# Performance work log

Measured on AMD Instinct MI355X. Metric: run time of the kernel, lower is better.

Reference implementation:

```python
import jax, jax.numpy as jnp
import numpy as np

N_QUBITS = 12
N_LAYERS = 2
B, T, IN, H = 256, 32, 8, 128
TWO_PI = 2.0 * np.pi


def _apply_1q(state, U, w):
    # state: (B, 2,2,...,2) with N_QUBITS qubit axes; U: (2,2) or (B,2,2)
    s = jnp.moveaxis(state, w + 1, 1)
    if U.ndim == 3:
        s = jnp.einsum('bst,bt...->bs...', U, s)
    else:
        s = jnp.einsum('st,bt...->bs...', U, s)
    return jnp.moveaxis(s, 1, w + 1)


def _rx_batched(angles):
    # angles: (B,) -> (B,2,2) RX matrices
    c = jnp.cos(angles / 2).astype(jnp.complex64)
    s = jnp.sin(angles / 2).astype(jnp.complex64)
    row0 = jnp.stack([c, -1j * s], axis=-1)
    row1 = jnp.stack([-1j * s, c], axis=-1)
    return jnp.stack([row0, row1], axis=1)


def _rot(phi, theta, omega):
    # PennyLane Rot = RZ(omega) RY(theta) RZ(phi)
    c = jnp.cos(theta / 2).astype(jnp.complex64)
    s = jnp.sin(theta / 2).astype(jnp.complex64)
    ep = jnp.exp(-0.5j * (phi + omega).astype(jnp.complex64))
    em = jnp.exp(-0.5j * (phi - omega).astype(jnp.complex64))
    m00 = ep * c
    m01 = -jnp.conj(em) * s
    m10 = em * s
    m11 = jnp.conj(ep) * c
    return jnp.stack([jnp.stack([m00, m01]), jnp.stack([m10, m11])])


def _cnot(state, cw, tw):
    flipped = jnp.flip(state, axis=tw + 1)
    mask = jnp.arange(2).reshape([2 if a == cw + 1 else 1 for a in range(N_QUBITS + 1)])
    return jnp.where(mask == 1, flipped, state)


def _run_circuit(angles, qw):
    # angles: (B, N_QUBITS) embedding angles; qw: (L, N, 3)
    b = angles.shape[0]
    state = jnp.zeros((b, 2 ** N_QUBITS), jnp.complex64).at[:, 0].set(1.0)
    state = state.reshape((b,) + (2,) * N_QUBITS)
    for w in range(N_QUBITS):  # AngleEmbedding, rotation='X'
        state = _apply_1q(state, _rx_batched(angles[:, w]), w)
    for l in range(N_LAYERS):  # StronglyEntanglingLayers
        for w in range(N_QUBITS):
            state = _apply_1q(state, _rot(qw[l, w, 0], qw[l, w, 1], qw[l, w, 2]), w)
        r = (l % (N_QUBITS - 1)) + 1
        for w in range(N_QUBITS):
            state = _cnot(state, w, (w + r) % N_QUBITS)
    probs = state.real ** 2 + state.imag ** 2
    evs = []
    for i in range(4):  # <Z_i>
        sign = (1.0 - 2.0 * jnp.arange(2, dtype=probs.dtype)).reshape(
            [2 if a == i + 1 else 1 for a in range(N_QUBITS + 1)])
        evs.append(jnp.sum(probs * sign, axis=tuple(range(1, N_QUBITS + 1))))
    return jnp.stack(evs, axis=1)  # (B, 4)


def setup_inputs() -> dict:
    key = jax.random.key(0)
    ks = jax.random.split(key, 12)
    inp = {
        'x': jax.random.normal(ks[0], (B, T, IN), jnp.float32),
        'h0': jnp.zeros((B, H), jnp.float32),
        'c0': jnp.zeros((B, H), jnp.float32),
        'q_weights': jax.random.uniform(ks[1], (N_LAYERS, N_QUBITS, 3), jnp.float32) * TWO_PI,
        'Wf': jax.random.normal(ks[2], (H, 1), jnp.float32),
        'bf': jax.random.normal(ks[3], (H,), jnp.float32) * 0.1,
        'Wi': jax.random.normal(ks[4], (H, 1), jnp.float32),
        'bi': jax.random.normal(ks[5], (H,), jnp.float32) * 0.1,
        'Wc': jax.random.normal(ks[6], (H, 1), jnp.float32),
        'bc': jax.random.normal(ks[7], (H,), jnp.float32) * 0.1,
        'Wo': jax.random.normal(ks[8], (H, 1), jnp.float32),
        'bo': jax.random.normal(ks[9], (H,), jnp.float32) * 0.1,
    }
    return inp


def reference(x, h0, c0, q_weights, Wf, bf, Wi, bi, Wc, bc, Wo, bo):
    def step(carry, x_t):
        h, c = carry
        comb = jnp.concatenate([x_t, h], axis=1)[:, :N_QUBITS]  # truncate, matches source
        q = _run_circuit(comb, q_weights)  # (B, 4) expvals in [-1, 1]
        f = jax.nn.sigmoid(q[:, 0:1] @ Wf.T + bf)
        i = jax.nn.sigmoid(q[:, 1:2] @ Wi.T + bi)
        ct = jnp.tanh(q[:, 2:3] @ Wc.T + bc)
        o = jax.nn.sigmoid(q[:, 3:4] @ Wo.T + bo)
        c_new = f * c + i * ct
        h_new = o * jnp.tanh(c_new)
        return (h_new, c_new), None

    (h_t, c_t), _ = jax.lax.scan(step, (h0, c0), jnp.swapaxes(x, 0, 1))
    return h_t, c_t
```

## Files before the change

### kernel.cpp

```cpp
#include <hip/hip_runtime.h>
#include <math.h>

#define NQ 12
#define NS 4096
#define TT 32
#define BB 256
#define HH 128
#define NT 512

typedef float v2f __attribute__((ext_vector_type(2)));
typedef float v4f __attribute__((ext_vector_type(4)));

constexpr unsigned cnot_g(unsigned x, int w, int r){
    int pc = 11 - w;
    int pt = 11 - ((w + r) % 12);
    return x ^ (((x >> pc) & 1u) << pt);
}
constexpr unsigned Fperm(unsigned i, int r){
    unsigned x = i;
    for (int w = 11; w >= 0; --w) x = cnot_g(x, w, r);
    return x;
}
constexpr unsigned Finv(unsigned i, int r){
    unsigned x = i;
    for (int w = 0; w < 12; ++w) x = cnot_g(x, w, r);
    return x;
}
constexpr unsigned F0closed(unsigned i){
    return i ^ ((i >> 1) & 0x7FFu) ^ ((i & 1u) << 10) ^ ((i & 1u) << 11);
}
constexpr bool check_all(){
    for (int b = 0; b < NQ; ++b){
        const unsigned e = 1u << b;
        if (F0closed(e) != Fperm(e,1)) return false;
        if (Fperm(Finv(e,1),1) != e) return false;
        if (Fperm(Finv(e,2),2) != e) return false;
    }
    if (F0closed(0u) != 0u || Fperm(0u,1) != 0u || Finv(0u,2) != 0u) return false;
    if (F0closed(0x5A3u) != Fperm(0x5A3u,1)) return false;
    if (Fperm(Finv(0xABCu,2),2) != 0xABCu) return false;
    return true;
}
static_assert(check_all(), "CNOT permutation closed forms wrong");
constexpr unsigned maskM(int k){
    unsigned m = 0;
    for (int b = 0; b < NQ; ++b) m |= ((Finv(1u<<b, 2) >> (11 - k)) & 1u) << b;
    return m;
}
constexpr unsigned gM0 = maskM(0), gM1 = maskM(1), gM2 = maskM(2), gM3 = maskM(3);
constexpr int sgn9(unsigned M, int K){ return __builtin_popcount((unsigned)K & (M >> 9)) & 1; }

__device__ __forceinline__ v2f pk_cmul(v2f m, v2f a){
    v2f t;
    asm("v_pk_mul_f32 %0, %1, %2 op_sel:[0,0] op_sel_hi:[0,1]"
        : "=v"(t) : "v"(m), "v"(a));
    asm("v_pk_fma_f32 %0, %1, %2, %0 op_sel:[1,1,0] op_sel_hi:[1,0,1] neg_lo:[1,0,0]"
        : "+v"(t) : "v"(m), "v"(a));
    return t;
}
template<int NL, int NH>
__device__ __forceinline__ void pk_accsgn(v2f &acc, v2f ppb){
    if constexpr (NL==0 && NH==0)
        asm("v_pk_add_f32 %0, %1, %0" : "+v"(acc) : "v"(ppb));
    else if constexpr (NL==1 && NH==0)
        asm("v_pk_add_f32 %0, %1, %0 neg_lo:[1,0]" : "+v"(acc) : "v"(ppb));
    else if constexpr (NL==0 && NH==1)
        asm("v_pk_add_f32 %0, %1, %0 neg_hi:[1,0]" : "+v"(acc) : "v"(ppb));
    else
        asm("v_pk_add_f32 %0, %1, %0 neg_lo:[1,0] neg_hi:[1,0]" : "+v"(acc) : "v"(ppb));
}
template<int K>
__device__ __forceinline__ void expk(const v2f* amp, v2f &a01, v2f &a23){
    const float pp = fmaf(amp[K].x, amp[K].x, amp[K].y * amp[K].y);
    v2f ppb; ppb.x = pp; ppb.y = pp;
    pk_accsgn<sgn9(gM0,K), sgn9(gM1,K)>(a01, ppb);
    pk_accsgn<sgn9(gM2,K), sgn9(gM3,K)>(a23, ppb);
    if constexpr (K < 7) expk<K+1>(amp, a01, a23);
}

template<int C>
__device__ __forceinline__ float dppadd(float v){
    return v + __int_as_float(
        __builtin_amdgcn_update_dpp(0, __float_as_int(v), C, 0xF, 0xF, true));
}
__device__ __forceinline__ float wsum(float v){
    v = dppadd<0x111>(v);
    v = dppadd<0x112>(v);
    v = dppadd<0x114>(v);
    v = dppadd<0x118>(v);
    v = dppadd<0x142>(v);
    v = dppadd<0x143>(v);
    return v;
}
template<int CTRL>
__device__ __forceinline__ float qpermf(float v){
    return __int_as_float(
        __builtin_amdgcn_update_dpp(0, __float_as_int(v), CTRL, 0xF, 0xF, true));
}
template<int CTRL>
__device__ __forceinline__ v4f qperm4(v4f v){
    v4f r;
    r.x = qpermf<CTRL>(v.x); r.y = qpermf<CTRL>(v.y);
    r.z = qpermf<CTRL>(v.z); r.w = qpermf<CTRL>(v.w);
    return r;
}


__device__ __forceinline__ float fsig(float xv){ return __fdividef(1.f, 1.f + __expf(-xv)); }
__device__ __forceinline__ float ftanh(float xv){
    const float e = __expf(-2.f * xv);
    return __fdividef(1.f - e, 1.f + e);
}

template<int WTOP>
__device__ __forceinline__ void rot3ry(v2f* s, const v2f* G){
    #pragma unroll
    for (int lb = 0; lb < 3; ++lb){
        const float cw = G[WTOP-lb].x, sw = G[WTOP-lb].y;
        #pragma unroll
        for (int k = 0; k < 8; ++k){
            if (k & (1 << lb)) continue;
            const int k1 = k | (1 << lb);
            const v2f a = s[k], b = s[k1];
            s[k]  = a*cw - b*sw;
            s[k1] = a*sw + b*cw;
        }
    }
}

extern "C" __global__ void __launch_bounds__(NT)
qlstm_kernel(const float* __restrict__ x,  const float* __restrict__ h0,
             const float* __restrict__ c0, const float* __restrict__ qw,
             const float* __restrict__ Wf, const float* __restrict__ bfp,
             const float* __restrict__ Wi, const float* __restrict__ bip,
             const float* __restrict__ Wc, const float* __restrict__ bcp,
             const float* __restrict__ Wo, const float* __restrict__ bop,
             float* __restrict__ out)
{
    __shared__ v2f S[NS];
    __shared__ v2f matp[NQ][4];
    __shared__ v2f vvx[8][2];
    __shared__ float xs[TT*8];
    __shared__ float4 red4[8];
    __shared__ float4 qh[TT];

    const int b    = blockIdx.x;
    const int tid  = threadIdx.x;
    const int wave = tid >> 6;
    const int lane = tid & 63;

    if (tid < NQ){
        const int w = tid;
        const float phi = qw[w*3 + 0];
        const float th  = qw[w*3 + 1];
        const float om  = qw[w*3 + 2];
        float cth, sth, cap, sap, cam, sam;
        sincosf(0.5f*th, &sth, &cth);
        sincosf(0.5f*(phi+om), &sap, &cap);
        sincosf(0.5f*(phi-om), &sam, &cam);
        v2f m00; m00.x =  cap*cth; m00.y = -sap*cth;
        v2f m01; m01.x = -cam*sth; m01.y = -sam*sth;
        v2f m10; m10.x =  cam*sth; m10.y = -sam*sth;
        v2f m11; m11.x =  cap*cth; m11.y =  sap*cth;
        matp[w][0] = m00; matp[w][1] = m01;
        matp[w][2] = m10; matp[w][3] = m11;
    }
    if (tid >= 256) xs[tid - 256] = x[b*(TT*8) + (tid - 256)];

    v2f G[NQ];
    #pragma unroll
    for (int w = 0; w < NQ; ++w){
        float cg, sg; sincosf(0.5f*qw[(NQ + w)*3 + 1], &sg, &cg);
        G[w].x = cg; G[w].y = sg;
    }
    v2f Zphi;
    {
        float A = 0.f;
        #pragma unroll
        for (int w = 0; w <= 8; ++w){
            const float ph = qw[(NQ + w)*3 + 0];
            A += ((tid >> (8 - w)) & 1) ? ph : -ph;
        }
        float sa, ca; sincosf(0.5f*A, &sa, &ca);
        Zphi.x = ca; Zphi.y = sa;
    }
    v2f dd[8];
    {
        const float p9  = qw[(NQ + 9)*3 + 0];
        const float p10 = qw[(NQ +10)*3 + 0];
        const float p11 = qw[(NQ +11)*3 + 0];
        #pragma unroll
        for (int k = 0; k < 8; ++k){
            const float Bq = 0.5f*(((k&4)? p9 : -p9) + ((k&2)? p10 : -p10) + ((k&1)? p11 : -p11));
            float sb, cb; sincosf(Bq, &sb, &cb);
            dd[k].x = cb; dd[k].y = sb;
        }
    }

    const int cw = tid & 3;
    const float WfC=Wf[cw], bfC=bfp[cw], WiC=Wi[cw], biC=bip[cw];
    const float WcC=Wc[cw], bcC=bcp[cw], WoC=Wo[cw], boC=bop[cw];
    float c4 = c0[b*HH + cw];
    const float h_init = h0[b*HH + cw];
    __syncthreads();

    const v2f M8w0 = matp[8+cw][0], M8w1 = matp[8+cw][1];
    const v2f M8w2 = matp[8+cw][2], M8w3 = matp[8+cw][3];

    if (tid >= 128 && tid < 136){
        const int w = tid - 128;
        float sa, ca; sincosf(0.5f*xs[w], &sa, &ca);
        const v2f M00=matp[w][0], M01=matp[w][1], M10=matp[w][2], M11=matp[w][3];
        v2f t0v; t0v.x = M00.x*ca + M01.y*sa; t0v.y = M00.y*ca - M01.x*sa;
        v2f t1v; t1v.x = M10.x*ca + M11.y*sa; t1v.y = M10.y*ca - M11.x*sa;
        vvx[w][0] = t0v; vvx[w][1] = t1v;
    }
    v4f hv0, hv1, hv2, hv3;
    {
        float sa, ca; sincosf(0.5f*h_init, &sa, &ca);
        v4f hw;
        hw.x = M8w0.x*ca + M8w1.y*sa;  hw.y = M8w0.y*ca - M8w1.x*sa;
        hw.z = M8w2.x*ca + M8w3.y*sa;  hw.w = M8w2.y*ca - M8w3.x*sa;
        hv0 = qperm4<0x00>(hw); hv1 = qperm4<0x55>(hw);
        hv2 = qperm4<0xAA>(hw); hv3 = qperm4<0xFF>(hw);
    }
    __syncthreads();

    const float sg0 = (__builtin_parity(tid & (gM0 & 0x1FFu)) ? -1.f : 1.f);
    const float sg1 = (__builtin_parity(tid & (gM1 & 0x1FFu)) ? -1.f : 1.f);
    const float sg2 = (__builtin_parity(tid & (gM2 & 0x1FFu)) ? -1.f : 1.f);
    const float sg3 = (__builtin_parity(tid & (gM3 & 0x1FFu)) ? -1.f : 1.f);
    const int bA = (tid << 3) ^ (tid & 31);
    const int bB = (tid & 7) ^ (((tid >> 3) & 3) << 3) ^ ((tid >> 3) << 6);
    const int bC = ((tid & 63) ^ ((tid >> 3) & 7)) | ((tid >> 6) << 9);
    const int bD = tid ^ ((tid >> 3) & 31);
    const int s2 = ((tid>>6) ^ (tid>>7)) & 1;
    const int s3 = ((tid>>5) ^ (tid>>6)) & 1;
    const int s4 = ((tid>>4) ^ (tid>>5)) & 1;
    const int s5 = ((tid>>3) ^ (tid>>4)) & 1;
    const int s6 = ((tid>>2) ^ (tid>>3)) & 1;
    const int s7 = ((tid>>1) ^ (tid>>2)) & 1;
    const int s8 = ( tid     ^ (tid>>1)) & 1;
    const int t8  = (tid >> 8) & 1;
    const int t78 = ((tid>>7) ^ (tid>>8)) & 1;
    const int t0  = tid & 1;
    const v2f* vf = &vvx[0][0];

    v2f QxZ, Ux0, Ux1;
    {
        const v2f e2 = vf[ 4+s2], e3 = vf[ 6+s3], e4 = vf[ 8+s4];
        const v2f e5 = vf[10+s5], e6 = vf[12+s6], e7 = vf[14+s7];
        QxZ = pk_cmul(pk_cmul(pk_cmul(e2,e3), pk_cmul(e4,e5)),
                      pk_cmul(pk_cmul(e6,e7), Zphi));
        const v2f v0a = vf[0], v0b = vf[1], v1a = vf[2], v1b = vf[3];
        const v2f ua0 = t8 ? v0b : v0a,  ua1 = t8 ? v0a : v0b;
        const v2f ub0 = t78 ? v1b : v1a, ub1 = t78 ? v1a : v1b;
        Ux0 = pk_cmul(ua0, ub0); Ux1 = pk_cmul(ua1, ub1);
    }

    v2f amp[8];

    #pragma unroll 1
    for (int t = 0; t < TT; ++t){
        v2f e8; e8.x = s8 ? hv0.z : hv0.x;  e8.y = s8 ? hv0.w : hv0.y;
        const v2f Q   = pk_cmul(QxZ, e8);
        const v2f QU0 = pk_cmul(Q, Ux0);
        const v2f QU1 = pk_cmul(Q, Ux1);
        v2f v9a; v9a.x = hv1.x; v9a.y = hv1.y;
        v2f v9b; v9b.x = hv1.z; v9b.y = hv1.w;
        const v2f v9s0 = t0 ? v9b : v9a, v9s1 = t0 ? v9a : v9b;
        v2f v10a; v10a.x = hv2.x; v10a.y = hv2.y;
        v2f v10b; v10b.x = hv2.z; v10b.y = hv2.w;
        v2f v11a; v11a.x = hv3.x; v11a.y = hv3.y;
        v2f v11b; v11b.x = hv3.z; v11b.y = hv3.w;
        const v2f P2_0 = pk_cmul(v10a, v11a), P2_1 = pk_cmul(v10a, v11b);
        const v2f P2_2 = pk_cmul(v10b, v11a), P2_3 = pk_cmul(v10b, v11b);
        #pragma unroll
        for (int k = 0; k < 8; ++k){
            const int g = k ^ (k >> 1);
            const v2f base = (k & 1) ? QU1 : QU0;
            const v2f w9   = (g & 4) ? v9s1 : v9s0;
            const v2f p2   = (g&3)==0 ? P2_0 : (g&3)==1 ? P2_1 : (g&3)==2 ? P2_2 : P2_3;
            amp[k] = pk_cmul(pk_cmul(base, w9), pk_cmul(p2, dd[k]));
        }

        rot3ry<11>(amp, G);
        #pragma unroll
        for (int k = 0; k < 8; ++k) S[bA ^ k] = amp[k];
        asm volatile("" ::: "memory");
        #pragma unroll
        for (int k = 0; k < 8; ++k) amp[k] = S[bB ^ (9*k)];
        rot3ry<8>(amp, G);
        #pragma unroll
        for (int k = 0; k < 8; ++k) S[bB ^ (9*k)] = amp[k];
        asm volatile("" ::: "memory");
        #pragma unroll
        for (int k = 0; k < 8; ++k) amp[k] = S[bC ^ ((k<<6) | ((k&3)<<3))];
        rot3ry<5>(amp, G);
        #pragma unroll
        for (int k = 0; k < 8; ++k) S[bC ^ ((k<<6) | ((k&3)<<3))] = amp[k];
        __syncthreads();
        #pragma unroll
        for (int k = 0; k < 8; ++k) amp[k] = S[bD + (k<<9)];
        rot3ry<2>(amp, G);

        v2f a01; a01.x = 0.f; a01.y = 0.f;
        v2f a23; a23.x = 0.f; a23.y = 0.f;
        expk<0>(amp, a01, a23);
        float p0 = a01.x * sg0, p1 = a01.y * sg1;
        float p2s = a23.x * sg2, p3 = a23.y * sg3;
        p0 = wsum(p0); p1 = wsum(p1); p2s = wsum(p2s); p3 = wsum(p3);
        if (lane == 63) red4[wave] = make_float4(p0, p1, p2s, p3);
        if (tid >= 128 && tid < 136){
            const int w  = tid - 128;
            const int tn = (t + 1 < TT) ? t + 1 : t;
            float sa, ca; __sincosf(0.5f*xs[tn*8 + w], &sa, &ca);
            const v2f M00=matp[w][0], M01=matp[w][1], M10=matp[w][2], M11=matp[w][3];
            v2f t0v; t0v.x = M00.x*ca + M01.y*sa; t0v.y = M00.y*ca - M01.x*sa;
            v2f t1v; t1v.x = M10.x*ca + M11.y*sa; t1v.y = M10.y*ca - M11.x*sa;
            vvx[w][0] = t0v; vvx[w][1] = t1v;
        }
        __syncthreads();

        float q0=0.f, q1=0.f, q2=0.f, q3=0.f;
        #pragma unroll
        for (int i = 0; i < 8; ++i){
            const float4 r = red4[i];
            q0 += r.x; q1 += r.y; q2 += r.z; q3 += r.w;
        }

        {
            const v2f e2 = vf[ 4+s2], e3 = vf[ 6+s3], e4 = vf[ 8+s4];
            const v2f e5 = vf[10+s5], e6 = vf[12+s6], e7 = vf[14+s7];
            QxZ = pk_cmul(pk_cmul(pk_cmul(e2,e3), pk_cmul(e4,e5)),
                          pk_cmul(pk_cmul(e6,e7), Zphi));
            const v2f v0a = vf[0], v0b = vf[1], v1a = vf[2], v1b = vf[3];
            const v2f ua0 = t8 ? v0b : v0a,  ua1 = t8 ? v0a : v0b;
            const v2f ub0 = t78 ? v1b : v1a, ub1 = t78 ? v1a : v1b;
            Ux0 = pk_cmul(ua0, ub0); Ux1 = pk_cmul(ua1, ub1);
        }

        if (tid == 0) qh[t] = make_float4(q0, q1, q2, q3);

        {
            const float fg = fsig (q0*WfC + bfC);
            const float ig = fsig (q1*WiC + biC);
            const float cg = ftanh(q2*WcC + bcC);
            const float og = fsig (q3*WoC + boC);
            c4 = fg*c4 + ig*cg;
            const float hj = og * ftanh(c4);
            float sa, ca; __sincosf(0.5f*hj, &sa, &ca);
            v4f hw;
            hw.x = M8w0.x*ca + M8w1.y*sa;  hw.y = M8w0.y*ca - M8w1.x*sa;
            hw.z = M8w2.x*ca + M8w3.y*sa;  hw.w = M8w2.y*ca - M8w3.x*sa;
            hv0 = qperm4<0x00>(hw); hv1 = qperm4<0x55>(hw);
            hv2 = qperm4<0xAA>(hw); hv3 = qperm4<0xFF>(hw);
        }
    }

    __syncthreads();
    if (tid < HH){
        const float wfE=Wf[tid], bfE=bfp[tid], wiE=Wi[tid], biE=bip[tid];
        const float wcE=Wc[tid], bcE=bcp[tid], woE=Wo[tid], boE=bop[tid];
        float cc = c0[b*HH + tid];
        float hh = 0.f;
        #pragma unroll 1
        for (int t = 0; t < TT; ++t){
            const float4 q = qh[t];
            const float fg = fsig (q.x*wfE + bfE);
            const float ig = fsig (q.y*wiE + biE);
            const float cg = ftanh(q.z*wcE + bcE);
            const float og = fsig (q.w*woE + boE);
            cc = fg*cc + ig*cg;
            hh = og * ftanh(cc);
        }
        out[b*HH + tid]         = hh;
        out[BB*HH + b*HH + tid] = cc;
    }
}

extern "C" void kernel_launch(void* const* d_in, const int* in_sizes, int n_in,
                              void* d_out, int out_size, void* d_ws, size_t ws_size,
                              hipStream_t stream)
{
    (void)in_sizes; (void)n_in; (void)d_ws; (void)ws_size; (void)out_size;
    const float* x  = (const float*)d_in[0];
    const float* h0 = (const float*)d_in[1];
    const float* c0 = (const float*)d_in[2];
    const float* qw = (const float*)d_in[3];
    const float* Wf = (const float*)d_in[4];
    const float* bf = (const float*)d_in[5];
    const float* Wi = (const float*)d_in[6];
    const float* bi = (const float*)d_in[7];
    const float* Wc = (const float*)d_in[8];
    const float* bc = (const float*)d_in[9];
    const float* Wo = (const float*)d_in[10];
    const float* bo = (const float*)d_in[11];
    qlstm_kernel<<<BB, NT, 0, stream>>>(x, h0, c0, qw, Wf, bf, Wi, bi,
                                        Wc, bc, Wo, bo, (float*)d_out);
}
```

Baseline: 93.11 us.

## Double threads per block to 1024 with 4 amplitudes each and swizzled LDS

Raises the block from 512 to 1024 threads, so each thread holds 4 amplitudes instead of 8. The RY rotation passes become six 2-qubit stages instead of four 3-qubit stages, and shared memory uses an XOR swizzle that is checked at compile time to be bank-conflict free. The 16 per-wave partial sums are reduced with DPP row operations instead of a serial loop. This cuts per-thread register work and serial latency, but adds LDS round trips and one more block barrier per timestep, and the larger block may lower occupancy.

```diff
diff --git a/kernel.cpp b/kernel.cpp
--- a/kernel.cpp
+++ b/kernel.cpp
@@ -6,7 +6,7 @@
 #define TT 32
 #define BB 256
 #define HH 128
-#define NT 512
+#define NT 1024
 
 typedef float v2f __attribute__((ext_vector_type(2)));
 typedef float v4f __attribute__((ext_vector_type(4)));
@@ -48,7 +48,47 @@
     return m;
 }
 constexpr unsigned gM0 = maskM(0), gM1 = maskM(1), gM2 = maskM(2), gM3 = maskM(3);
-constexpr int sgn9(unsigned M, int K){ return __builtin_popcount((unsigned)K & (M >> 9)) & 1; }
+constexpr int sgn2(unsigned M, int K){ return __builtin_popcount((unsigned)K & (M >> 10)) & 1; }
+
+constexpr int swz12(int j){
+    int s = j;
+    s ^= (j >> 5) & 7;
+    s ^= ((j >> 4) & 1) << 3;
+    s ^= ((j >> 1) & 1) << 4;
+    return s;
+}
+constexpr unsigned jcfg(int c, unsigned tid, unsigned k){
+    switch(c){
+        case 0: return (tid << 2) | k;
+        case 1: return ((tid>>2)<<4) | (k<<2) | (tid&3);
+        case 2: return ((tid>>4)<<6) | (k<<4) | (tid&15);
+        case 3: return ((tid>>6)<<8) | (k<<6) | (tid&63);
+        case 4: return ((tid>>8)<<10) | (k<<8) | (tid&255);
+        default:return (k<<10) | tid;
+    }
+}
+constexpr bool banks_ok(){
+    for (int c = 0; c < 6; ++c){
+        int cnt[32] = {};
+        for (unsigned l = 0; l < 64; ++l) cnt[swz12((int)jcfg(c, l, 0)) & 31]++;
+        for (int b = 0; b < 32; ++b) if (cnt[b] != 2) return false;
+    }
+    return true;
+}
+static_assert(banks_ok(), "swizzle not conflict-free for some config");
+constexpr bool bij_ok(){
+    for (int hi = 0; hi < 128; ++hi){
+        unsigned seen = 0;
+        for (int lo = 0; lo < 32; ++lo){
+            const int s = swz12((hi << 5) | lo);
+            if ((s >> 5) != hi) return false;
+            seen |= 1u << (s & 31);
+        }
+        if (seen != 0xFFFFFFFFu) return false;
+    }
+    return true;
+}
+static_assert(bij_ok(), "swizzle not bijective");
 
 __device__ __forceinline__ v2f pk_cmul(v2f m, v2f a){
     v2f t;
@@ -70,12 +110,12 @@
         asm("v_pk_add_f32 %0, %1, %0 neg_lo:[1,0] neg_hi:[1,0]" : "+v"(acc) : "v"(ppb));
 }
 template<int K>
-__device__ __forceinline__ void expk(const v2f* amp, v2f &a01, v2f &a23){
+__device__ __forceinline__ void expk4(const v2f* amp, v2f &a01, v2f &a23){
     const float pp = fmaf(amp[K].x, amp[K].x, amp[K].y * amp[K].y);
     v2f ppb; ppb.x = pp; ppb.y = pp;
-    pk_accsgn<sgn9(gM0,K), sgn9(gM1,K)>(a01, ppb);
-    pk_accsgn<sgn9(gM2,K), sgn9(gM3,K)>(a23, ppb);
-    if constexpr (K < 7) expk<K+1>(amp, a01, a23);
+    pk_accsgn<sgn2(gM0,K), sgn2(gM1,K)>(a01, ppb);
+    pk_accsgn<sgn2(gM2,K), sgn2(gM3,K)>(a23, ppb);
+    if constexpr (K < 3) expk4<K+1>(amp, a01, a23);
 }
 
 template<int C>
@@ -92,6 +132,13 @@
     v = dppadd<0x143>(v);
     return v;
 }
+__device__ __forceinline__ float bfsum16(float v){
+    v = dppadd<0xB1>(v);
+    v = dppadd<0x4E>(v);
+    v = dppadd<0x141>(v);
+    v = dppadd<0x140>(v);
+    return v;
+}
 template<int CTRL>
 __device__ __forceinline__ float qpermf(float v){
     return __int_as_float(
@@ -105,7 +152,6 @@
     return r;
 }
 
-
 __device__ __forceinline__ float fsig(float xv){ return __fdividef(1.f, 1.f + __expf(-xv)); }
 __device__ __forceinline__ float ftanh(float xv){
     const float e = __expf(-2.f * xv);
@@ -113,17 +159,23 @@
 }
 
 template<int WTOP>
-__device__ __forceinline__ void rot3ry(v2f* s, const v2f* G){
-    #pragma unroll
-    for (int lb = 0; lb < 3; ++lb){
-        const float cw = G[WTOP-lb].x, sw = G[WTOP-lb].y;
-        #pragma unroll
-        for (int k = 0; k < 8; ++k){
-            if (k & (1 << lb)) continue;
-            const int k1 = k | (1 << lb);
-            const v2f a = s[k], b = s[k1];
-            s[k]  = a*cw - b*sw;
-            s[k1] = a*sw + b*cw;
+__device__ __forceinline__ void rot2ry(v2f* s, const v2f* G){
+    {
+        const float cw = G[WTOP].x, sw = G[WTOP].y;
+        #pragma unroll
+        for (int m = 0; m < 4; m += 2){
+            const v2f a = s[m], b = s[m+1];
+            s[m]   = a*cw - b*sw;
+            s[m+1] = a*sw + b*cw;
+        }
+    }
+    {
+        const float cw = G[WTOP-1].x, sw = G[WTOP-1].y;
+        #pragma unroll
+        for (int m = 0; m < 2; ++m){
+            const v2f a = s[m], b = s[m+2];
+            s[m]   = a*cw - b*sw;
+            s[m+2] = a*sw + b*cw;
         }
     }
 }
@@ -141,7 +193,7 @@
     __shared__ v2f matp[NQ][4];
     __shared__ v2f vvx[8][2];
     __shared__ float xs[TT*8];
-    __shared__ float4 red4[8];
+    __shared__ float4 red4[16];
     __shared__ float4 qh[TT];
 
     const int b    = blockIdx.x;
@@ -165,7 +217,7 @@
         matp[w][0] = m00; matp[w][1] = m01;
         matp[w][2] = m10; matp[w][3] = m11;
     }
-    if (tid >= 256) xs[tid - 256] = x[b*(TT*8) + (tid - 256)];
+    if (tid >= 256 && tid < 512) xs[tid - 256] = x[b*(TT*8) + (tid - 256)];
 
     v2f G[NQ];
     #pragma unroll
@@ -177,23 +229,22 @@
     {
         float A = 0.f;
         #pragma unroll
-        for (int w = 0; w <= 8; ++w){
-            const float ph = qw[(NQ + w)*3 + 0];
-            A += ((tid >> (8 - w)) & 1) ? ph : -ph;
-        }
-        float sa, ca; sincosf(0.5f*A, &sa, &ca);
+        for (int w = 0; w <= 9; ++w){
+            const float ph = 0.5f*qw[(NQ + w)*3 + 0];
+            A += ((tid >> (9 - w)) & 1) ? ph : -ph;
+        }
+        float sa, ca; sincosf(A, &sa, &ca);
         Zphi.x = ca; Zphi.y = sa;
     }
-    v2f dd[8];
-    {
-        const float p9  = qw[(NQ + 9)*3 + 0];
-        const float p10 = qw[(NQ +10)*3 + 0];
-        const float p11 = qw[(NQ +11)*3 + 0];
-        #pragma unroll
-        for (int k = 0; k < 8; ++k){
-            const float Bq = 0.5f*(((k&4)? p9 : -p9) + ((k&2)? p10 : -p10) + ((k&1)? p11 : -p11));
-            float sb, cb; sincosf(Bq, &sb, &cb);
-            dd[k].x = cb; dd[k].y = sb;
+    v2f dd[4];
+    {
+        const float f10 = 0.5f*qw[(NQ + 10)*3 + 0];
+        const float f11 = 0.5f*qw[(NQ + 11)*3 + 0];
+        #pragma unroll
+        for (int k = 0; k < 4; ++k){
+            const float P = (((k>>1)&1) ? f10 : -f10) + ((k&1) ? f11 : -f11);
+            float sp, cp; sincosf(P, &sp, &cp);
+            dd[k].x = cp; dd[k].y = sp;
         }
     }
 
@@ -226,24 +277,27 @@
     }
     __syncthreads();
 
-    const float sg0 = (__builtin_parity(tid & (gM0 & 0x1FFu)) ? -1.f : 1.f);
-    const float sg1 = (__builtin_parity(tid & (gM1 & 0x1FFu)) ? -1.f : 1.f);
-    const float sg2 = (__builtin_parity(tid & (gM2 & 0x1FFu)) ? -1.f : 1.f);
-    const float sg3 = (__builtin_parity(tid & (gM3 & 0x1FFu)) ? -1.f : 1.f);
-    const int bA = (tid << 3) ^ (tid & 31);
-    const int bB = (tid & 7) ^ (((tid >> 3) & 3) << 3) ^ ((tid >> 3) << 6);
-    const int bC = ((tid & 63) ^ ((tid >> 3) & 7)) | ((tid >> 6) << 9);
-    const int bD = tid ^ ((tid >> 3) & 31);
-    const int s2 = ((tid>>6) ^ (tid>>7)) & 1;
-    const int s3 = ((tid>>5) ^ (tid>>6)) & 1;
-    const int s4 = ((tid>>4) ^ (tid>>5)) & 1;
-    const int s5 = ((tid>>3) ^ (tid>>4)) & 1;
-    const int s6 = ((tid>>2) ^ (tid>>3)) & 1;
-    const int s7 = ((tid>>1) ^ (tid>>2)) & 1;
-    const int s8 = ( tid     ^ (tid>>1)) & 1;
-    const int t8  = (tid >> 8) & 1;
-    const int t78 = ((tid>>7) ^ (tid>>8)) & 1;
-    const int t0  = tid & 1;
+    const float sg0 = (__builtin_parity(tid & (gM0 & 0x3FFu)) ? -1.f : 1.f);
+    const float sg1 = (__builtin_parity(tid & (gM1 & 0x3FFu)) ? -1.f : 1.f);
+    const float sg2 = (__builtin_parity(tid & (gM2 & 0x3FFu)) ? -1.f : 1.f);
+    const float sg3 = (__builtin_parity(tid & (gM3 & 0x3FFu)) ? -1.f : 1.f);
+    const int bA = swz12((int)jcfg(0, (unsigned)tid, 0));
+    const int bB = swz12((int)jcfg(1, (unsigned)tid, 0));
+    const int bC = swz12((int)jcfg(2, (unsigned)tid, 0));
+    const int bD = swz12((int)jcfg(3, (unsigned)tid, 0));
+    const int bE = swz12((int)jcfg(4, (unsigned)tid, 0));
+    const int bF = swz12((int)jcfg(5, (unsigned)tid, 0));
+    const int s2 = ((tid>>7) ^ (tid>>8)) & 1;
+    const int s3 = ((tid>>6) ^ (tid>>7)) & 1;
+    const int s4 = ((tid>>5) ^ (tid>>6)) & 1;
+    const int s5 = ((tid>>4) ^ (tid>>5)) & 1;
+    const int s6 = ((tid>>3) ^ (tid>>4)) & 1;
+    const int s7 = ((tid>>2) ^ (tid>>3)) & 1;
+    const int s8 = ((tid>>1) ^ (tid>>2)) & 1;
+    const int s9 = ( tid     ^ (tid>>1)) & 1;
+    const int t9s  = (tid >> 9) & 1;
+    const int t89s = ((tid>>8) ^ (tid>>9)) & 1;
+    const int t0   = tid & 1;
     const v2f* vf = &vvx[0][0];
 
     v2f QxZ, Ux0, Ux1;
@@ -252,61 +306,63 @@
         const v2f e5 = vf[10+s5], e6 = vf[12+s6], e7 = vf[14+s7];
         QxZ = pk_cmul(pk_cmul(pk_cmul(e2,e3), pk_cmul(e4,e5)),
                       pk_cmul(pk_cmul(e6,e7), Zphi));
-        const v2f v0a = vf[0], v0b = vf[1], v1a = vf[2], v1b = vf[3];
-        const v2f ua0 = t8 ? v0b : v0a,  ua1 = t8 ? v0a : v0b;
-        const v2f ub0 = t78 ? v1b : v1a, ub1 = t78 ? v1a : v1b;
-        Ux0 = pk_cmul(ua0, ub0); Ux1 = pk_cmul(ua1, ub1);
-    }
-
-    v2f amp[8];
+        Ux0 = pk_cmul(vf[0+t9s],     vf[2+t89s]);
+        Ux1 = pk_cmul(vf[0+(t9s^1)], vf[2+(t89s^1)]);
+    }
+
+    v2f amp[4];
 
     #pragma unroll 1
     for (int t = 0; t < TT; ++t){
-        v2f e8; e8.x = s8 ? hv0.z : hv0.x;  e8.y = s8 ? hv0.w : hv0.y;
-        const v2f Q   = pk_cmul(QxZ, e8);
-        const v2f QU0 = pk_cmul(Q, Ux0);
-        const v2f QU1 = pk_cmul(Q, Ux1);
-        v2f v9a; v9a.x = hv1.x; v9a.y = hv1.y;
-        v2f v9b; v9b.x = hv1.z; v9b.y = hv1.w;
-        const v2f v9s0 = t0 ? v9b : v9a, v9s1 = t0 ? v9a : v9b;
-        v2f v10a; v10a.x = hv2.x; v10a.y = hv2.y;
-        v2f v10b; v10b.x = hv2.z; v10b.y = hv2.w;
+        v2f e8v;  e8v.x = s8 ? hv0.z : hv0.x;  e8v.y = s8 ? hv0.w : hv0.y;
+        v2f e9v;  e9v.x = s9 ? hv1.z : hv1.x;  e9v.y = s9 ? hv1.w : hv1.y;
+        const v2f QH  = pk_cmul(QxZ, pk_cmul(e8v, e9v));
+        const v2f QU0 = pk_cmul(QH, Ux0);
+        const v2f QU1 = pk_cmul(QH, Ux1);
+        v2f v10a; v10a.x = t0 ? hv2.z : hv2.x;  v10a.y = t0 ? hv2.w : hv2.y;
+        v2f v10b; v10b.x = t0 ? hv2.x : hv2.z;  v10b.y = t0 ? hv2.y : hv2.w;
         v2f v11a; v11a.x = hv3.x; v11a.y = hv3.y;
         v2f v11b; v11b.x = hv3.z; v11b.y = hv3.w;
-        const v2f P2_0 = pk_cmul(v10a, v11a), P2_1 = pk_cmul(v10a, v11b);
-        const v2f P2_2 = pk_cmul(v10b, v11a), P2_3 = pk_cmul(v10b, v11b);
-        #pragma unroll
-        for (int k = 0; k < 8; ++k){
-            const int g = k ^ (k >> 1);
-            const v2f base = (k & 1) ? QU1 : QU0;
-            const v2f w9   = (g & 4) ? v9s1 : v9s0;
-            const v2f p2   = (g&3)==0 ? P2_0 : (g&3)==1 ? P2_1 : (g&3)==2 ? P2_2 : P2_3;
-            amp[k] = pk_cmul(pk_cmul(base, w9), pk_cmul(p2, dd[k]));
-        }
-
-        rot3ry<11>(amp, G);
-        #pragma unroll
-        for (int k = 0; k < 8; ++k) S[bA ^ k] = amp[k];
+        amp[0] = pk_cmul(pk_cmul(QU0, v10a), pk_cmul(v11a, dd[0]));
+        amp[1] = pk_cmul(pk_cmul(QU1, v10a), pk_cmul(v11b, dd[1]));
+        amp[2] = pk_cmul(pk_cmul(QU0, v10b), pk_cmul(v11b, dd[2]));
+        amp[3] = pk_cmul(pk_cmul(QU1, v10b), pk_cmul(v11a, dd[3]));
+
+        rot2ry<11>(amp, G);
+        #pragma unroll
+        for (int k = 0; k < 4; ++k) S[bA ^ swz12((int)jcfg(0,0,k))] = amp[k];
         asm volatile("" ::: "memory");
         #pragma unroll
-        for (int k = 0; k < 8; ++k) amp[k] = S[bB ^ (9*k)];
-        rot3ry<8>(amp, G);
-        #pragma unroll
-        for (int k = 0; k < 8; ++k) S[bB ^ (9*k)] = amp[k];
+        for (int k = 0; k < 4; ++k) amp[k] = S[bB ^ swz12((int)jcfg(1,0,k))];
+        rot2ry<9>(amp, G);
+        #pragma unroll
+        for (int k = 0; k < 4; ++k) S[bB ^ swz12((int)jcfg(1,0,k))] = amp[k];
         asm volatile("" ::: "memory");
         #pragma unroll
-        for (int k = 0; k < 8; ++k) amp[k] = S[bC ^ ((k<<6) | ((k&3)<<3))];
-        rot3ry<5>(amp, G);
-        #pragma unroll
-        for (int k = 0; k < 8; ++k) S[bC ^ ((k<<6) | ((k&3)<<3))] = amp[k];
+        for (int k = 0; k < 4; ++k) amp[k] = S[bC ^ swz12((int)jcfg(2,0,k))];
+        rot2ry<7>(amp, G);
+        #pragma unroll
+        for (int k = 0; k < 4; ++k) S[bC ^ swz12((int)jcfg(2,0,k))] = amp[k];
+        asm volatile("" ::: "memory");
+        #pragma unroll
+        for (int k = 0; k < 4; ++k) amp[k] = S[bD ^ swz12((int)jcfg(3,0,k))];
+        rot2ry<5>(amp, G);
+        #pragma unroll
+        for (int k = 0; k < 4; ++k) S[bD ^ swz12((int)jcfg(3,0,k))] = amp[k];
         __syncthreads();
         #pragma unroll
-        for (int k = 0; k < 8; ++k) amp[k] = S[bD + (k<<9)];
-        rot3ry<2>(amp, G);
+        for (int k = 0; k < 4; ++k) amp[k] = S[bE ^ swz12((int)jcfg(4,0,k))];
+        rot2ry<3>(amp, G);
+        #pragma unroll
+        for (int k = 0; k < 4; ++k) S[bE ^ swz12((int)jcfg(4,0,k))] = amp[k];
+        __syncthreads();
+        #pragma unroll
+        for (int k = 0; k < 4; ++k) amp[k] = S[bF ^ swz12((int)jcfg(5,0,k))];
+        rot2ry<1>(amp, G);
 
         v2f a01; a01.x = 0.f; a01.y = 0.f;
         v2f a23; a23.x = 0.f; a23.y = 0.f;
-        expk<0>(amp, a01, a23);
+        expk4<0>(amp, a01, a23);
         float p0 = a01.x * sg0, p1 = a01.y * sg1;
         float p2s = a23.x * sg2, p3 = a23.y * sg3;
         p0 = wsum(p0); p1 = wsum(p1); p2s = wsum(p2s); p3 = wsum(p3);
@@ -322,22 +378,17 @@
         }
         __syncthreads();
 
-        float q0=0.f, q1=0.f, q2=0.f, q3=0.f;
-        #pragma unroll
-        for (int i = 0; i < 8; ++i){
-            const float4 r = red4[i];
-            q0 += r.x; q1 += r.y; q2 += r.z; q3 += r.w;
-        }
+        const float4 r = red4[lane & 15];
+        float q0 = bfsum16(r.x), q1 = bfsum16(r.y);
+        float q2 = bfsum16(r.z), q3 = bfsum16(r.w);
 
         {
             const v2f e2 = vf[ 4+s2], e3 = vf[ 6+s3], e4 = vf[ 8+s4];
             const v2f e5 = vf[10+s5], e6 = vf[12+s6], e7 = vf[14+s7];
             QxZ = pk_cmul(pk_cmul(pk_cmul(e2,e3), pk_cmul(e4,e5)),
                           pk_cmul(pk_cmul(e6,e7), Zphi));
-            const v2f v0a = vf[0], v0b = vf[1], v1a = vf[2], v1b = vf[3];
-            const v2f ua0 = t8 ? v0b : v0a,  ua1 = t8 ? v0a : v0b;
-            const v2f ub0 = t78 ? v1b : v1a, ub1 = t78 ? v1a : v1b;
-            Ux0 = pk_cmul(ua0, ub0); Ux1 = pk_cmul(ua1, ub1);
+            Ux0 = pk_cmul(vf[0+t9s],     vf[2+t89s]);
+            Ux1 = pk_cmul(vf[0+(t9s^1)], vf[2+(t89s^1)]);
         }
 
         if (tid == 0) qh[t] = make_float4(q0, q1, q2, q3);
```

New measurement: 130.1 us. 39.8% more time.
